# Optimization experiments

Hardware: AMD Instinct MI355X
Metric: run time of the kernel (lower is better)

Reference implementation:

```python
import jax, jax.numpy as jnp
import numpy as np

DIM = 512

def setup_inputs() -> dict:
    key = jax.random.key(0)
    ks = jax.random.split(key, 8)
    B, T, S, D = 4, 128, 512, DIM
    scale = 1.0 / np.sqrt(D)
    return {
        "inp": jax.random.normal(ks[0], (B, T, D), jnp.float32),
        "context": jax.random.normal(ks[1], (B, S, D), jnp.float32),
        # linear_query: Linear(D, D, bias=True)
        "Wq": jax.random.normal(ks[2], (D, D), jnp.float32) * scale,
        "bq": jax.random.normal(ks[3], (D,), jnp.float32) * scale,
        # linear_context: Linear(D, D, bias=False)
        "Wc": jax.random.normal(ks[4], (D, D), jnp.float32) * scale,
        # v: Linear(D, 1, bias=False)
        "v": jax.random.normal(ks[5], (D,), jnp.float32) * scale,
        # linear_out: Linear(2D, D, bias=True)
        "Wout": jax.random.normal(ks[6], (D, 2 * D), jnp.float32) * scale,
        "bout": jax.random.normal(ks[7], (D,), jnp.float32) * scale,
    }

def reference(inp, context, Wq, bq, Wc, v, Wout, bout):
    # inp: (B,T,D) target queries; context: (B,S,D) source states
    wq = jnp.einsum('btd,ed->bte', inp, Wq) + bq          # (B,T,D)
    uh = jnp.einsum('bsd,ed->bse', context, Wc)            # (B,S,D)
    # additive (Bahdanau) score: v^T tanh(Wq q_t + Wc h_s)
    wquh = jnp.tanh(wq[:, :, None, :] + uh[:, None, :, :])  # (B,T,S,D)
    align = jnp.einsum('btsd,d->bts', wquh, v)             # (B,T,S)
    align_vectors = jax.nn.softmax(align, axis=-1)          # softmax over src_len
    c = jnp.einsum('bts,bsd->btd', align_vectors, context)  # context vector
    concat_c = jnp.concatenate([c, inp], axis=-1)           # (B,T,2D)
    attn_h = jnp.einsum('btf,ef->bte', concat_c, Wout) + bout  # (B,T,D)
    return attn_h, align_vectors
```

## Files before the change

kernel.cpp:

```cpp
#include <hip/hip_runtime.h>
#include <hip/hip_bf16.h>
#include <math.h>


typedef __attribute__((ext_vector_type(8))) short short8;
typedef __attribute__((ext_vector_type(4))) float f32x4;
typedef unsigned short ushort_t;

static __device__ __forceinline__ unsigned short f2bf(float x) {
    union { __hip_bfloat16 h; unsigned short u; } c;
    c.h = __float2bfloat16(x);
    return c.u;
}
static __device__ __forceinline__ int bf2x(float lo, float hi) {
    return (int)(((unsigned)f2bf(hi) << 16) | (unsigned)f2bf(lo));
}

template<bool BF>
static __device__ __forceinline__ void load16(const void* base, size_t elemoff,
                                              int4& r0, int4& r1) {
    if (BF) {
        const int4* p = (const int4*)((const ushort_t*)base + elemoff);
        r0 = p[0]; r1 = p[1];
    } else {
        const float4* p = (const float4*)((const float*)base + elemoff);
        float4 a = p[0], b = p[1], c = p[2], d = p[3];
        r0.x = bf2x(a.x, a.y); r0.y = bf2x(a.z, a.w);
        r0.z = bf2x(b.x, b.y); r0.w = bf2x(b.z, b.w);
        r1.x = bf2x(c.x, c.y); r1.y = bf2x(c.z, c.w);
        r1.z = bf2x(d.x, d.y); r1.w = bf2x(d.z, d.w);
    }
}

template<bool A_BF, bool W_BF, int EPI>
static __device__ __forceinline__ void gemm_body(
    ushort_t* As, ushort_t* Ws,
    const void* A, const void* W, const float* bias, const float* partial,
    void* Cv, int K, int lda, int ldw, int ldc, int bm, int bn)
{
    const int tid = threadIdx.x;
    const int wave = tid >> 6, lane = tid & 63;
    const int mh = (wave & 1) * 32, nh = (wave >> 1) * 32;
    const int quad = lane >> 4, l16 = lane & 15;
    const int srow = tid >> 2, schunk = tid & 3;

    const size_t aoff = (size_t)(bm + srow) * lda + schunk * 16;
    const size_t woff = (size_t)(bn + srow) * ldw + schunk * 16;
    int4* AsW = (int4*)&As[srow * 72 + schunk * 16];
    int4* WsW = (int4*)&Ws[srow * 72 + schunk * 16];

    f32x4 acc00 = {0.f, 0.f, 0.f, 0.f}, acc01 = acc00, acc10 = acc00, acc11 = acc00;

    int4 a0r, a1r, w0r, w1r;
    load16<A_BF>(A, aoff, a0r, a1r);
    load16<W_BF>(W, woff, w0r, w1r);

    for (int k0 = 0; k0 < K; k0 += 64) {
        AsW[0] = a0r; AsW[1] = a1r;
        WsW[0] = w0r; WsW[1] = w1r;
        __syncthreads();
        if (k0 + 64 < K) {
            load16<A_BF>(A, aoff + k0 + 64, a0r, a1r);
            load16<W_BF>(W, woff + k0 + 64, w0r, w1r);
        }
        #pragma unroll
        for (int kk = 0; kk < 64; kk += 32) {
            short8 a0 = *(const short8*)&As[(mh + l16) * 72 + kk + quad * 8];
            short8 a1 = *(const short8*)&As[(mh + 16 + l16) * 72 + kk + quad * 8];
            short8 b0 = *(const short8*)&Ws[(nh + l16) * 72 + kk + quad * 8];
            short8 b1 = *(const short8*)&Ws[(nh + 16 + l16) * 72 + kk + quad * 8];
            acc00 = __builtin_amdgcn_mfma_f32_16x16x32_bf16(a0, b0, acc00, 0, 0, 0);
            acc01 = __builtin_amdgcn_mfma_f32_16x16x32_bf16(a0, b1, acc01, 0, 0, 0);
            acc10 = __builtin_amdgcn_mfma_f32_16x16x32_bf16(a1, b0, acc10, 0, 0, 0);
            acc11 = __builtin_amdgcn_mfma_f32_16x16x32_bf16(a1, b1, acc11, 0, 0, 0);
        }
        __syncthreads();
    }

    const int col0 = bn + nh + l16;
    const int col1 = col0 + 16;
    float bias0 = bias ? bias[col0] : 0.f;
    float bias1 = bias ? bias[col1] : 0.f;

    f32x4 accs[2][2] = {{acc00, acc01}, {acc10, acc11}};
    #pragma unroll
    for (int mt = 0; mt < 2; ++mt) {
        #pragma unroll
        for (int r = 0; r < 4; ++r) {
            int row = bm + mh + mt * 16 + quad * 4 + r;
            size_t rowoff = (size_t)row * ldc;
            float v0 = accs[mt][0][r] + bias0;
            float v1 = accs[mt][1][r] + bias1;
            if (EPI == 1) { v0 = __expf(2.f * v0); v1 = __expf(2.f * v1); }
            if (EPI == 3) { v0 += partial[rowoff + col0]; v1 += partial[rowoff + col1]; }
            if (EPI == 2) {
                ushort_t* C = (ushort_t*)Cv;
                C[rowoff + col0] = f2bf(v0);
                C[rowoff + col1] = f2bf(v1);
            } else {
                float* C = (float*)Cv;
                C[rowoff + col0] = v0;
                C[rowoff + col1] = v1;
            }
        }
    }
}

__global__ __launch_bounds__(256) void cvt_bf16(
    const float* __restrict__ inp, const float* __restrict__ ctx,
    const float* __restrict__ Wq, const float* __restrict__ Wc,
    const float* __restrict__ Wout,
    ushort_t* __restrict__ inpb, ushort_t* __restrict__ ctxb,
    ushort_t* __restrict__ Wqb, ushort_t* __restrict__ Wcb,
    ushort_t* __restrict__ Woutb)
{
    const int bid = blockIdx.x;
    const float* src; ushort_t* dst; int base;
    if (bid < 128)      { src = inp;  dst = inpb;  base = bid; }
    else if (bid < 640) { src = ctx;  dst = ctxb;  base = bid - 128; }
    else if (bid < 768) { src = Wq;   dst = Wqb;   base = bid - 640; }
    else if (bid < 896) { src = Wc;   dst = Wcb;   base = bid - 768; }
    else                { src = Wout; dst = Woutb; base = bid - 896; }
    const size_t off = (size_t)base * 2048 + (size_t)threadIdx.x * 8;
    const float4* s = (const float4*)(src + off);
    float4 a = s[0], b = s[1];
    int4 r;
    r.x = bf2x(a.x, a.y); r.y = bf2x(a.z, a.w);
    r.z = bf2x(b.x, b.y); r.w = bf2x(b.z, b.w);
    *(int4*)(dst + off) = r;
}

__global__ __launch_bounds__(256) void fused_front(
    const ushort_t* __restrict__ inpb, const ushort_t* __restrict__ ctxb,
    const ushort_t* __restrict__ Wqb, const float* __restrict__ bq,
    const ushort_t* __restrict__ Wcb, const ushort_t* __restrict__ Woutb,
    const float* __restrict__ bout,
    float* __restrict__ Ew, float* __restrict__ Eu, float* __restrict__ Y0,
    ushort_t* __restrict__ GT)
{
    __shared__ ushort_t As[64 * 72];
    __shared__ ushort_t Ws[64 * 72];
    const int bid = blockIdx.x;

    if (bid < 64) {
        gemm_body<true, true, 1>(As, Ws, inpb, Wqb, bq, nullptr, Ew,
                                 512, 512, 512, 512, (bid & 7) * 64, (bid >> 3) * 64);
    } else if (bid < 320) {
        int i = bid - 64;
        gemm_body<true, true, 1>(As, Ws, ctxb, Wcb, nullptr, nullptr, Eu,
                                 512, 512, 512, 512, (i & 31) * 64, (i >> 5) * 64);
    } else if (bid < 576) {
        int i = bid - 320;
        int b = i >> 6, j = i & 63;
        gemm_body<true, true, 2>(As, Ws, Woutb, ctxb + (size_t)b * 262144, nullptr,
                                 nullptr, GT + (size_t)b * 262144,
                                 512, 1024, 512, 512, (j & 7) * 64, (j >> 3) * 64);
    } else {
        int i = bid - 576;
        gemm_body<true, true, 0>(As, Ws, inpb, Woutb + 512, bout, nullptr, Y0,
                                 512, 512, 1024, 512, (i & 7) * 64, (i >> 3) * 64);
    }
}

__global__ __launch_bounds__(256) void align_kernel(
    const float* __restrict__ Ew, const float* __restrict__ Eu,
    const float* __restrict__ v, float* __restrict__ out)
{
    const int lane = threadIdx.x & 63, wave = threadIdx.x >> 6;
    const int b = blockIdx.z;
    const int t0 = blockIdx.y * 16 + wave * 4;
    const int s0 = blockIdx.x * 8;

    const float* wp = Ew + (((size_t)(b * 128 + t0)) << 9);
    const float* up = Eu + (((size_t)(b * 512 + s0)) << 9);

    float acc[4][8];
    #pragma unroll
    for (int i = 0; i < 4; ++i)
        #pragma unroll
        for (int j = 0; j < 8; ++j) acc[i][j] = 0.f;
    float vsum = 0.f;

    for (int k0 = 0; k0 < 512; k0 += 128) {
        float va = v[k0 + lane];
        float vb = v[k0 + 64 + lane];
        vsum += va + vb;
        float wa[4], wb[4];
        #pragma unroll
        for (int i = 0; i < 4; ++i) {
            wa[i] = wp[i * 512 + k0 + lane];
            wb[i] = wp[i * 512 + k0 + 64 + lane];
        }
        #pragma unroll
        for (int j = 0; j < 8; ++j) {
            const float* u = up + ((size_t)j << 9) + k0 + lane;
            float ua = u[0];
            float ub = u[64];
            #pragma unroll
            for (int i = 0; i < 4; ++i) {
                float A = fmaf(wa[i], ua, 1.f);
                float B = fmaf(wb[i], ub, 1.f);
                float num = fmaf(va, B, vb * A);
                float r = __builtin_amdgcn_rcpf(A * B);
                acc[i][j] = fmaf(num, r, acc[i][j]);
            }
        }
    }

    float V = vsum;
    #pragma unroll
    for (int off = 32; off; off >>= 1) V += __shfl_xor(V, off, 64);

    float x16[16];
    {
        const bool hb = lane & 1;
        #pragma unroll
        for (int i = 0; i < 4; ++i)
            #pragma unroll
            for (int m = 0; m < 4; ++m) {
                float keep = hb ? acc[i][2 * m + 1] : acc[i][2 * m];
                float send = hb ? acc[i][2 * m]     : acc[i][2 * m + 1];
                x16[i * 4 + m] = keep + __shfl_xor(send, 1, 64);
            }
    }
    float x8[8];
    {
        const bool hb = lane & 2;
        #pragma unroll
        for (int m = 0; m < 8; ++m) {
            float keep = hb ? x16[2 * m + 1] : x16[2 * m];
            float send = hb ? x16[2 * m]     : x16[2 * m + 1];
            x8[m] = keep + __shfl_xor(send, 2, 64);
        }
    }
    float x4[4];
    {
        const bool hb = lane & 4;
        #pragma unroll
        for (int m = 0; m < 4; ++m) {
            float keep = hb ? x8[2 * m + 1] : x8[2 * m];
            float send = hb ? x8[2 * m]     : x8[2 * m + 1];
            x4[m] = keep + __shfl_xor(send, 4, 64);
        }
    }
    float x2[2];
    {
        const bool hb = lane & 8;
        #pragma unroll
        for (int m = 0; m < 2; ++m) {
            float keep = hb ? x4[2 * m + 1] : x4[2 * m];
            float send = hb ? x4[2 * m]     : x4[2 * m + 1];
            x2[m] = keep + __shfl_xor(send, 8, 64);
        }
    }
    float x1;
    {
        const bool hb = lane & 16;
        float keep = hb ? x2[1] : x2[0];
        float send = hb ? x2[0] : x2[1];
        x1 = keep + __shfl_xor(send, 16, 64);
    }
    x1 += __shfl_xor(x1, 32, 64);

    const int oi = (lane >> 3) & 3;
    const int oj = lane & 7;
    float e = __expf(fmaf(-2.f, x1, V));
    if (lane < 32) {
        out[(((size_t)(b * 128 + t0 + oi)) << 9) + s0 + oj] = e;
    }
}

__global__ __launch_bounds__(256) void normalize_512(
    const float* __restrict__ E, float* __restrict__ alignv,
    ushort_t* __restrict__ pbf)
{
    const int row = blockIdx.x;
    const float* p = E + ((size_t)row << 9);
    float* a = alignv + ((size_t)row << 9);
    ushort_t* q = pbf + ((size_t)row << 9);
    const int tid = threadIdx.x;
    float e0 = p[tid];
    float e1 = p[tid + 256];

    float s = e0 + e1;
    #pragma unroll
    for (int off = 32; off > 0; off >>= 1)
        s += __shfl_xor(s, off, 64);
    __shared__ float reds[4];
    const int wave = tid >> 6;
    if ((tid & 63) == 0) reds[wave] = s;
    __syncthreads();
    s = (reds[0] + reds[1]) + (reds[2] + reds[3]);
    float r = 1.0f / s;
    float p0 = e0 * r, p1 = e1 * r;
    a[tid] = p0;
    a[tid + 256] = p1;
    q[tid] = f2bf(p0);
    q[tid + 256] = f2bf(p1);
}

__global__ __launch_bounds__(256) void gemm_att(
    const ushort_t* __restrict__ P, const ushort_t* __restrict__ GT,
    const float* __restrict__ Y0, float* __restrict__ attn)
{
    __shared__ ushort_t As[64 * 72];
    __shared__ ushort_t Ws[64 * 72];
    const int b = blockIdx.z;
    gemm_body<true, true, 3>(As, Ws,
                             P + (size_t)b * 65536, GT + (size_t)b * 262144,
                             nullptr, Y0 + (size_t)b * 65536,
                             attn + (size_t)b * 65536,
                             512, 512, 512, 512, blockIdx.x * 64, blockIdx.y * 64);
}

extern "C" void kernel_launch(void* const* d_in, const int* in_sizes, int n_in,
                              void* d_out, int out_size, void* d_ws, size_t ws_size,
                              hipStream_t stream)
{
    const float* inp  = (const float*)d_in[0];
    const float* ctx  = (const float*)d_in[1];
    const float* Wq   = (const float*)d_in[2];
    const float* bq   = (const float*)d_in[3];
    const float* Wc   = (const float*)d_in[4];
    const float* v    = (const float*)d_in[5];
    const float* Wout = (const float*)d_in[6];
    const float* bout = (const float*)d_in[7];

    float* out    = (float*)d_out;
    float* attn   = out;
    float* alignv = out + 262144;

    float* ws = (float*)d_ws;
    float* Ew   = ws;
    float* Eu   = ws + 262144;
    float* Y0   = ws + 1310720;
    float* E    = ws + 1572864;
    ushort_t* GT   = (ushort_t*)(ws + 1835008);
    ushort_t* P_bf = (ushort_t*)(ws + 2359296);
    ushort_t* inpb  = (ushort_t*)(ws + 2490368);
    ushort_t* ctxb  = (ushort_t*)(ws + 2621440);
    ushort_t* Wqb   = (ushort_t*)(ws + 3145728);
    ushort_t* Wcb   = (ushort_t*)(ws + 3276800);
    ushort_t* Woutb = (ushort_t*)(ws + 3407872);

    cvt_bf16<<<dim3(1152), 256, 0, stream>>>(inp, ctx, Wq, Wc, Wout,
                                             inpb, ctxb, Wqb, Wcb, Woutb);
    fused_front<<<dim3(640), 256, 0, stream>>>(inpb, ctxb, Wqb, bq, Wcb, Woutb,
                                               bout, Ew, Eu, Y0, GT);
    align_kernel<<<dim3(64, 8, 4), 256, 0, stream>>>(Ew, Eu, v, E);
    normalize_512<<<dim3(512), 256, 0, stream>>>(E, alignv, P_bf);
    gemm_att<<<dim3(2, 8, 4), 256, 0, stream>>>(P_bf, GT, Y0, attn);
}
```

Before: 110.3 us.

## Use direct global-to-LDS loads with swizzled double-buffered GEMM tiles

Replaces the register-staged GEMM tile loads with global_load_lds 16-byte transfers straight into LDS. Padded rows give way to an XOR-swizzled 64-wide layout that avoids bank conflicts. The shared buffers are doubled so the next K-tile loads while the current one is consumed, which drops one barrier per iteration. This removes register round-trips and a sync, but doubles LDS use per block and relies on the barrier waiting for the async LDS loads to finish.

```diff
diff --git a/kernel.cpp b/kernel.cpp
--- a/kernel.cpp
+++ b/kernel.cpp
@@ -16,65 +16,68 @@
     return (int)(((unsigned)f2bf(hi) << 16) | (unsigned)f2bf(lo));
 }
 
-template<bool BF>
-static __device__ __forceinline__ void load16(const void* base, size_t elemoff,
-                                              int4& r0, int4& r1) {
-    if (BF) {
-        const int4* p = (const int4*)((const ushort_t*)base + elemoff);
-        r0 = p[0]; r1 = p[1];
-    } else {
-        const float4* p = (const float4*)((const float*)base + elemoff);
-        float4 a = p[0], b = p[1], c = p[2], d = p[3];
-        r0.x = bf2x(a.x, a.y); r0.y = bf2x(a.z, a.w);
-        r0.z = bf2x(b.x, b.y); r0.w = bf2x(b.z, b.w);
-        r1.x = bf2x(c.x, c.y); r1.y = bf2x(c.z, c.w);
-        r1.z = bf2x(d.x, d.y); r1.w = bf2x(d.z, d.w);
-    }
-}
-
-template<bool A_BF, bool W_BF, int EPI>
+static __device__ __forceinline__ void gld16(const ushort_t* g, ushort_t* l) {
+    __builtin_amdgcn_global_load_lds(
+        (const __attribute__((address_space(1))) unsigned int*)g,
+        (__attribute__((address_space(3))) unsigned int*)l, 16, 0, 0);
+}
+
+template<int EPI>
 static __device__ __forceinline__ void gemm_body(
     ushort_t* As, ushort_t* Ws,
-    const void* A, const void* W, const float* bias, const float* partial,
+    const ushort_t* A, const ushort_t* W,
+    const float* bias, const float* partial,
     void* Cv, int K, int lda, int ldw, int ldc, int bm, int bn)
 {
     const int tid = threadIdx.x;
     const int wave = tid >> 6, lane = tid & 63;
     const int mh = (wave & 1) * 32, nh = (wave >> 1) * 32;
     const int quad = lane >> 4, l16 = lane & 15;
-    const int srow = tid >> 2, schunk = tid & 3;
-
-    const size_t aoff = (size_t)(bm + srow) * lda + schunk * 16;
-    const size_t woff = (size_t)(bn + srow) * ldw + schunk * 16;
-    int4* AsW = (int4*)&As[srow * 72 + schunk * 16];
-    int4* WsW = (int4*)&Ws[srow * 72 + schunk * 16];
+
+    const int sr0 = 8 * wave + (lane >> 3);
+    const int sc  = (((lane & 7) ^ (sr0 & 7)) << 3);
+    const size_t ga0 = (size_t)(bm + sr0) * lda + sc;
+    const size_t ga1 = (size_t)(bm + sr0 + 32) * lda + sc;
+    const size_t gw0 = (size_t)(bn + sr0) * ldw + sc;
+    const size_t gw1 = (size_t)(bn + sr0 + 32) * ldw + sc;
+    ushort_t* al0 = As + wave * 512;
+    ushort_t* al1 = As + 2048 + wave * 512;
+    ushort_t* wl0 = Ws + wave * 512;
+    ushort_t* wl1 = Ws + 2048 + wave * 512;
 
     f32x4 acc00 = {0.f, 0.f, 0.f, 0.f}, acc01 = acc00, acc10 = acc00, acc11 = acc00;
 
-    int4 a0r, a1r, w0r, w1r;
-    load16<A_BF>(A, aoff, a0r, a1r);
-    load16<W_BF>(W, woff, w0r, w1r);
-
+    gld16(A + ga0, al0);
+    gld16(A + ga1, al1);
+    gld16(W + gw0, wl0);
+    gld16(W + gw1, wl1);
+
+    const int swz = l16 & 7;
+    int cur = 0;
     for (int k0 = 0; k0 < K; k0 += 64) {
-        AsW[0] = a0r; AsW[1] = a1r;
-        WsW[0] = w0r; WsW[1] = w1r;
         __syncthreads();
         if (k0 + 64 < K) {
-            load16<A_BF>(A, aoff + k0 + 64, a0r, a1r);
-            load16<W_BF>(W, woff + k0 + 64, w0r, w1r);
-        }
-        #pragma unroll
-        for (int kk = 0; kk < 64; kk += 32) {
-            short8 a0 = *(const short8*)&As[(mh + l16) * 72 + kk + quad * 8];
-            short8 a1 = *(const short8*)&As[(mh + 16 + l16) * 72 + kk + quad * 8];
-            short8 b0 = *(const short8*)&Ws[(nh + l16) * 72 + kk + quad * 8];
-            short8 b1 = *(const short8*)&Ws[(nh + 16 + l16) * 72 + kk + quad * 8];
+            const int nb = (cur ^ 1) * 4096;
+            gld16(A + ga0 + k0 + 64, al0 + nb);
+            gld16(A + ga1 + k0 + 64, al1 + nb);
+            gld16(W + gw0 + k0 + 64, wl0 + nb);
+            gld16(W + gw1 + k0 + 64, wl1 + nb);
+        }
+        const ushort_t* Ab = As + cur * 4096;
+        const ushort_t* Wb = Ws + cur * 4096;
+        #pragma unroll
+        for (int kc = 0; kc < 8; kc += 4) {
+            const int ch = ((quad + kc) ^ swz) << 3;
+            short8 a0 = *(const short8*)&Ab[(mh + l16) * 64 + ch];
+            short8 a1 = *(const short8*)&Ab[(mh + 16 + l16) * 64 + ch];
+            short8 b0 = *(const short8*)&Wb[(nh + l16) * 64 + ch];
+            short8 b1 = *(const short8*)&Wb[(nh + 16 + l16) * 64 + ch];
             acc00 = __builtin_amdgcn_mfma_f32_16x16x32_bf16(a0, b0, acc00, 0, 0, 0);
             acc01 = __builtin_amdgcn_mfma_f32_16x16x32_bf16(a0, b1, acc01, 0, 0, 0);
             acc10 = __builtin_amdgcn_mfma_f32_16x16x32_bf16(a1, b0, acc10, 0, 0, 0);
             acc11 = __builtin_amdgcn_mfma_f32_16x16x32_bf16(a1, b1, acc11, 0, 0, 0);
         }
-        __syncthreads();
+        cur ^= 1;
     }
 
     const int col0 = bn + nh + l16;
@@ -138,27 +141,27 @@
     float* __restrict__ Ew, float* __restrict__ Eu, float* __restrict__ Y0,
     ushort_t* __restrict__ GT)
 {
-    __shared__ ushort_t As[64 * 72];
-    __shared__ ushort_t Ws[64 * 72];
+    __shared__ ushort_t As[2 * 4096];
+    __shared__ ushort_t Ws[2 * 4096];
     const int bid = blockIdx.x;
 
     if (bid < 64) {
-        gemm_body<true, true, 1>(As, Ws, inpb, Wqb, bq, nullptr, Ew,
-                                 512, 512, 512, 512, (bid & 7) * 64, (bid >> 3) * 64);
+        gemm_body<1>(As, Ws, inpb, Wqb, bq, nullptr, Ew,
+                     512, 512, 512, 512, (bid & 7) * 64, (bid >> 3) * 64);
     } else if (bid < 320) {
         int i = bid - 64;
-        gemm_body<true, true, 1>(As, Ws, ctxb, Wcb, nullptr, nullptr, Eu,
-                                 512, 512, 512, 512, (i & 31) * 64, (i >> 5) * 64);
+        gemm_body<1>(As, Ws, ctxb, Wcb, nullptr, nullptr, Eu,
+                     512, 512, 512, 512, (i & 31) * 64, (i >> 5) * 64);
     } else if (bid < 576) {
         int i = bid - 320;
         int b = i >> 6, j = i & 63;
-        gemm_body<true, true, 2>(As, Ws, Woutb, ctxb + (size_t)b * 262144, nullptr,
-                                 nullptr, GT + (size_t)b * 262144,
-                                 512, 1024, 512, 512, (j & 7) * 64, (j >> 3) * 64);
+        gemm_body<2>(As, Ws, Woutb, ctxb + (size_t)b * 262144, nullptr,
+                     nullptr, GT + (size_t)b * 262144,
+                     512, 1024, 512, 512, (j & 7) * 64, (j >> 3) * 64);
     } else {
         int i = bid - 576;
-        gemm_body<true, true, 0>(As, Ws, inpb, Woutb + 512, bout, nullptr, Y0,
-                                 512, 512, 1024, 512, (i & 7) * 64, (i >> 3) * 64);
+        gemm_body<0>(As, Ws, inpb, Woutb + 512, bout, nullptr, Y0,
+                     512, 512, 1024, 512, (i & 7) * 64, (i >> 3) * 64);
     }
 }
 
@@ -303,14 +306,14 @@
     const ushort_t* __restrict__ P, const ushort_t* __restrict__ GT,
     const float* __restrict__ Y0, float* __restrict__ attn)
 {
-    __shared__ ushort_t As[64 * 72];
-    __shared__ ushort_t Ws[64 * 72];
+    __shared__ ushort_t As[2 * 4096];
+    __shared__ ushort_t Ws[2 * 4096];
     const int b = blockIdx.z;
-    gemm_body<true, true, 3>(As, Ws,
-                             P + (size_t)b * 65536, GT + (size_t)b * 262144,
-                             nullptr, Y0 + (size_t)b * 65536,
-                             attn + (size_t)b * 65536,
-                             512, 512, 512, 512, blockIdx.x * 64, blockIdx.y * 64);
+    gemm_body<3>(As, Ws,
+                 P + (size_t)b * 65536, GT + (size_t)b * 262144,
+                 nullptr, Y0 + (size_t)b * 65536,
+                 attn + (size_t)b * 65536,
+                 512, 512, 512, 512, blockIdx.x * 64, blockIdx.y * 64);
 }
 
 extern "C" void kernel_launch(void* const* d_in, const int* in_sizes, int n_in,
```

Result: slower. 113.2 us (+2.7%).
